# Optimization experiments

Measured on AMD Instinct MI355X. Metric: run time of the kernel, lower is better.

## Reference

```python
import jax, jax.numpy as jnp
import numpy as np

N = 100000   # nodes
E = 3200000  # edges (before self-loops)


def _glorot(k, fi, fo):
    lim = np.sqrt(6.0 / (fi + fo)).astype(np.float32)
    return jax.random.uniform(k, (fi, fo), jnp.float32, -lim, lim)


def setup_inputs() -> dict:
    key = jax.random.key(0)
    ks = jax.random.split(key, 8)
    x = jax.random.normal(ks[0], (N, 128), jnp.float32)
    edge_index = jax.random.randint(ks[1], (2, E), 0, N, dtype=jnp.int32)
    return {
        "x": x,
        "edge_index": edge_index,
        "W1": _glorot(ks[2], 128, 64), "b1": jnp.zeros((64,), jnp.float32),
        "W2": _glorot(ks[3], 64, 32),  "b2": jnp.zeros((32,), jnp.float32),
        "W3": _glorot(ks[4], 32, 16),  "b3": jnp.zeros((16,), jnp.float32),
        "Wl": _glorot(ks[5], 16, 4),   "bl": jnp.zeros((4,), jnp.float32),
    }


def _gcn_layer(h_in, W, b, src, dst, norm, n):
    # PyG GCNConv: x' = D^-1/2 (A+I) D^-1/2 (x W) + b
    h = h_in @ W                                   # [N, out]
    msg = h[src] * norm[:, None]                   # gather + normalize, [E+N, out]
    out = jax.ops.segment_sum(msg, dst, num_segments=n)
    return out + b


def reference(x, edge_index, W1, b1, W2, b2, W3, b3, Wl, bl):
    n = x.shape[0]
    loops = jnp.arange(n, dtype=edge_index.dtype)
    src = jnp.concatenate([edge_index[0], loops])  # source nodes (messages flow src->dst)
    dst = jnp.concatenate([edge_index[1], loops])
    # symmetric gcn_norm with self-loops (edge_weight = 1)
    deg = jax.ops.segment_sum(jnp.ones_like(dst, dtype=x.dtype), dst, num_segments=n)
    dinv = jnp.where(deg > 0, jax.lax.rsqrt(deg), 0.0)
    norm = dinv[src] * dinv[dst]                   # [E+N]

    h = jax.nn.relu(_gcn_layer(x, W1, b1, src, dst, norm, n))
    h = jax.nn.relu(_gcn_layer(h, W2, b2, src, dst, norm, n))
    h = jax.nn.relu(_gcn_layer(h, W3, b3, src, dst, norm, n))
    z = h @ Wl + bl
    return (h, z)
```

## Files before the change

### kernel.cpp

```cpp
#include <hip/hip_runtime.h>

static constexpr int BLK = 256;
static constexpr int BW_SHIFT = 8;
static constexpr int NBUCK_MAX = 512;
static constexpr int CAP = 12288;


__device__ inline float bflo(unsigned u) {
    union { unsigned x; float f; } c; c.x = u << 16; return c.f;
}
__device__ inline float bfhi(unsigned u) {
    union { unsigned x; float f; } c; c.x = u & 0xFFFF0000u; return c.f;
}
__device__ inline unsigned short f2bf(float f) {
    union { float f; unsigned u; } c; c.f = f;
    unsigned u = c.u;
    return (unsigned short)((u + 0x7FFFu + ((u >> 16) & 1u)) >> 16);
}
__device__ inline unsigned pack2(float a, float b) {
    return (unsigned)f2bf(a) | ((unsigned)f2bf(b) << 16);
}


__global__ __launch_bounds__(1024) void k_part(
        const int* __restrict__ src, const int* __restrict__ dst,
        int* __restrict__ bcur, int* __restrict__ pairs, int e, int nbuck) {
    __shared__ int hcnt[NBUCK_MAX];
    __shared__ int hbase[NBUCK_MAX];
    const int nt = blockDim.x;
    int nblk = gridDim.x;
    int per = (e + nblk - 1) / nblk;
    int lo = blockIdx.x * per, hi = min(e, lo + per);
    for (int i = threadIdx.x; i < nbuck; i += nt) hcnt[i] = 0;
    __syncthreads();
    for (int i = lo + threadIdx.x; i < hi; i += nt)
        atomicAdd(&hcnt[dst[i] >> BW_SHIFT], 1);
    __syncthreads();
    for (int i = threadIdx.x; i < nbuck; i += nt) {
        int c = hcnt[i];
        hbase[i] = c ? atomicAdd(bcur + i, c) : 0;
        hcnt[i] = 0;
    }
    __syncthreads();
    for (int i = lo + threadIdx.x; i < hi; i += nt) {
        int d = dst[i];
        int b = d >> BW_SHIFT;
        int pos = hbase[b] + atomicAdd(&hcnt[b], 1);
        if (pos < CAP)
            pairs[(size_t)b * CAP + pos] = src[i] | ((d & 255) << 24);
    }
}


__global__ void k_bktscan(const int* __restrict__ bcur, int* __restrict__ bktbase,
                          int* __restrict__ row_ptr, int nbuck, int n, int e) {
    __shared__ int s[512];
    int v = ((int)threadIdx.x < nbuck) ? bcur[threadIdx.x] : 0;
    s[threadIdx.x] = v;
    __syncthreads();
    for (int off = 1; off < 512; off <<= 1) {
        int t = (threadIdx.x >= (unsigned)off) ? s[threadIdx.x - off] : 0;
        __syncthreads();
        s[threadIdx.x] += t;
        __syncthreads();
    }
    if ((int)threadIdx.x < nbuck)
        bktbase[threadIdx.x] = s[threadIdx.x] - v;
    if (threadIdx.x == 0) row_ptr[n] = e;
}


__global__ __launch_bounds__(512) void k_bucket_build(
        const int* __restrict__ pairs, const int* __restrict__ bcur,
        const int* __restrict__ bktbase, int* __restrict__ row_ptr,
        float* __restrict__ dinv, int* __restrict__ csr, int n) {
    __shared__ int lcnt[256];
    __shared__ int sexc[256];
    const int b = blockIdx.x;
    const int node0 = b << BW_SHIFT;
    const int nn = min(256, n - node0);
    const int cnt = min(bcur[b], CAP);
    const int base = bktbase[b];
    const int* bp = pairs + (size_t)b * CAP;
    const int tid = threadIdx.x;
    const int nt = blockDim.x;

    if (tid < 256) lcnt[tid] = 0;
    __syncthreads();
    for (int i = tid; i < cnt; i += nt)
        atomicAdd(&lcnt[(unsigned)bp[i] >> 24], 1);
    __syncthreads();
    int c = 0;
    if (tid < 256) {
        c = lcnt[tid];
        sexc[tid] = c;
    }
    __syncthreads();
    for (int off = 1; off < 256; off <<= 1) {
        int t = 0;
        if (tid < 256 && tid >= off) t = sexc[tid - off];
        __syncthreads();
        if (tid < 256) sexc[tid] += t;
        __syncthreads();
    }
    if (tid < nn) {
        int excl = sexc[tid] - c;
        row_ptr[node0 + tid] = base + excl;
        dinv[node0 + tid] = rsqrtf((float)(c + 1));
    }
    __syncthreads();
    if (tid < 256) {
        sexc[tid] -= c;
        lcnt[tid] = 0;
    }
    __syncthreads();
    for (int i = tid; i < cnt; i += nt) {
        int pv = bp[i];
        int ld = (unsigned)pv >> 24;
        int pos = base + sexc[ld] + atomicAdd(&lcnt[ld], 1);
        csr[pos] = pv & 0xFFFFFF;
    }
}


template <int K, int F>
__global__ __launch_bounds__(256) void k_gemm_tiled(const float* __restrict__ X,
                                                    const float* __restrict__ W,
                                                    const float* __restrict__ dinv,
                                                    unsigned short* __restrict__ G,
                                                    int n) {
    constexpr int KT = 32;
    constexpr int TF = F / 16;
    static_assert(K % KT == 0, "");
    __shared__ float xs[KT][68];
    __shared__ float wsm[KT * F];
    const int tid = threadIdx.x;
    const int ng = tid & 15;
    const int fg = tid >> 4;
    const int node0 = blockIdx.x * 64;

    float acc[4][TF];
#pragma unroll
    for (int m = 0; m < 4; ++m)
#pragma unroll
        for (int j = 0; j < TF; ++j) acc[m][j] = 0.0f;

    for (int kt = 0; kt < K / KT; ++kt) {
#pragma unroll
        for (int v = 0; v < 2; ++v) {
            int fi = tid + v * 256;
            int nd = fi >> 3, kq = fi & 7;
            int row = min(node0 + nd, n - 1);
            float4 xv = *(const float4*)&X[(size_t)row * K + kt * KT + kq * 4];
            xs[kq * 4 + 0][nd] = xv.x;
            xs[kq * 4 + 1][nd] = xv.y;
            xs[kq * 4 + 2][nd] = xv.z;
            xs[kq * 4 + 3][nd] = xv.w;
        }
        constexpr int WV = KT * F / 4;
        for (int fi = tid; fi < WV; fi += 256)
            ((float4*)wsm)[fi] = ((const float4*)(W + (size_t)kt * KT * F))[fi];
        __syncthreads();

#pragma unroll 8
        for (int kk = 0; kk < KT; ++kk) {
            float4 xv = *(const float4*)&xs[kk][ng * 4];
            float wv[TF];
#pragma unroll
            for (int j = 0; j < TF; ++j) wv[j] = wsm[kk * F + fg * TF + j];
            const float xm[4] = {xv.x, xv.y, xv.z, xv.w};
#pragma unroll
            for (int m = 0; m < 4; ++m)
#pragma unroll
                for (int j = 0; j < TF; ++j) acc[m][j] = fmaf(xm[m], wv[j], acc[m][j]);
        }
        __syncthreads();
    }

#pragma unroll
    for (int m = 0; m < 4; ++m) {
        int node = node0 + ng * 4 + m;
        if (node < n) {
            float di = dinv[node];
            unsigned short* gp = G + (size_t)node * F + fg * TF;
            if constexpr (TF == 4) {
                uint2 o;
                o.x = pack2(acc[m][0] * di, acc[m][1] * di);
                o.y = pack2(acc[m][2] * di, acc[m][3] * di);
                *(uint2*)gp = o;
            } else if constexpr (TF == 2) {
                *(unsigned*)gp = pack2(acc[m][0] * di, acc[m][1] * di);
            } else {
                gp[0] = f2bf(acc[m][0] * di);
            }
        }
    }
}


template <int F, bool HEAD>
__global__ void k_agg(const int* __restrict__ row_ptr, const int* __restrict__ csr,
                      const uint4* __restrict__ g4, const float* __restrict__ dinv,
                      const float* __restrict__ b, float* __restrict__ out, int n,
                      const float* __restrict__ Wl, const float* __restrict__ blp,
                      float* __restrict__ z_out) {
    constexpr int L = F / 8;
    constexpr int NPB = BLK / L;
    __shared__ float wl_s[68];
    if constexpr (HEAD) {
        if (threadIdx.x < 68)
            wl_s[threadIdx.x] = (threadIdx.x < 64) ? Wl[threadIdx.x]
                                                   : blp[threadIdx.x - 64];
        __syncthreads();
    }
    int node = blockIdx.x * NPB + (int)(threadIdx.x / L);
    int q = threadIdx.x % L;
    if (node >= n) return;
    int i = row_ptr[node], end = row_ptr[node + 1];
    float a[8];
#pragma unroll
    for (int j = 0; j < 8; ++j) a[j] = 0.0f;
    for (; i + 3 < end; i += 4) {
        int s0 = csr[i], s1 = csr[i + 1], s2 = csr[i + 2], s3 = csr[i + 3];
        uint4 v0 = g4[(size_t)s0 * L + q];
        uint4 v1 = g4[(size_t)s1 * L + q];
        uint4 v2 = g4[(size_t)s2 * L + q];
        uint4 v3 = g4[(size_t)s3 * L + q];
        a[0] += (bflo(v0.x) + bflo(v1.x)) + (bflo(v2.x) + bflo(v3.x));
        a[1] += (bfhi(v0.x) + bfhi(v1.x)) + (bfhi(v2.x) + bfhi(v3.x));
        a[2] += (bflo(v0.y) + bflo(v1.y)) + (bflo(v2.y) + bflo(v3.y));
        a[3] += (bfhi(v0.y) + bfhi(v1.y)) + (bfhi(v2.y) + bfhi(v3.y));
        a[4] += (bflo(v0.z) + bflo(v1.z)) + (bflo(v2.z) + bflo(v3.z));
        a[5] += (bfhi(v0.z) + bfhi(v1.z)) + (bfhi(v2.z) + bfhi(v3.z));
        a[6] += (bflo(v0.w) + bflo(v1.w)) + (bflo(v2.w) + bflo(v3.w));
        a[7] += (bfhi(v0.w) + bfhi(v1.w)) + (bfhi(v2.w) + bfhi(v3.w));
    }
    for (; i < end; ++i) {
        uint4 v = g4[(size_t)csr[i] * L + q];
        a[0] += bflo(v.x); a[1] += bfhi(v.x);
        a[2] += bflo(v.y); a[3] += bfhi(v.y);
        a[4] += bflo(v.z); a[5] += bfhi(v.z);
        a[6] += bflo(v.w); a[7] += bfhi(v.w);
    }
    uint4 vs = g4[(size_t)node * L + q];
    a[0] += bflo(vs.x); a[1] += bfhi(vs.x);
    a[2] += bflo(vs.y); a[3] += bfhi(vs.y);
    a[4] += bflo(vs.z); a[5] += bfhi(vs.z);
    a[6] += bflo(vs.w); a[7] += bfhi(vs.w);

    float di = dinv[node];
    float4 b0 = ((const float4*)b)[2 * q];
    float4 b1 = ((const float4*)b)[2 * q + 1];
    float h[8];
    h[0] = fmaxf(fmaf(di, a[0], b0.x), 0.0f);
    h[1] = fmaxf(fmaf(di, a[1], b0.y), 0.0f);
    h[2] = fmaxf(fmaf(di, a[2], b0.z), 0.0f);
    h[3] = fmaxf(fmaf(di, a[3], b0.w), 0.0f);
    h[4] = fmaxf(fmaf(di, a[4], b1.x), 0.0f);
    h[5] = fmaxf(fmaf(di, a[5], b1.y), 0.0f);
    h[6] = fmaxf(fmaf(di, a[6], b1.z), 0.0f);
    h[7] = fmaxf(fmaf(di, a[7], b1.w), 0.0f);
    float4* op = (float4*)out + (size_t)node * (F / 4) + 2 * q;
    op[0] = make_float4(h[0], h[1], h[2], h[3]);
    op[1] = make_float4(h[4], h[5], h[6], h[7]);

    if constexpr (HEAD) {
        float p[4];
#pragma unroll
        for (int j = 0; j < 4; ++j) p[j] = 0.0f;
#pragma unroll
        for (int k = 0; k < 8; ++k) {
            const float hv = h[k];
            const int kr = (q * 8 + k) * 4;
#pragma unroll
            for (int j = 0; j < 4; ++j) p[j] = fmaf(hv, wl_s[kr + j], p[j]);
        }
#pragma unroll
        for (int j = 0; j < 4; ++j) p[j] += __shfl_xor(p[j], 1);
        if (q == 0) {
            float4 zt = make_float4(p[0] + wl_s[64], p[1] + wl_s[65],
                                    p[2] + wl_s[66], p[3] + wl_s[67]);
            ((float4*)z_out)[node] = zt;
        }
    }
}


extern "C" void kernel_launch(void* const* d_in, const int* in_sizes, int n_in,
                              void* d_out, int out_size, void* d_ws, size_t ws_size,
                              hipStream_t stream) {
    const float* x  = (const float*)d_in[0];
    const int*   ei = (const int*)d_in[1];
    const float* W1 = (const float*)d_in[2];
    const float* b1 = (const float*)d_in[3];
    const float* W2 = (const float*)d_in[4];
    const float* b2 = (const float*)d_in[5];
    const float* W3 = (const float*)d_in[6];
    const float* b3 = (const float*)d_in[7];
    const float* Wl = (const float*)d_in[8];
    const float* bl = (const float*)d_in[9];

    const int n = in_sizes[0] / 128;
    const int e = in_sizes[1] / 2;
    const int* src = ei;
    const int* dst = ei + e;

    const int nbuck = (n + (1 << BW_SHIFT) - 1) >> BW_SHIFT;

    char* ws = (char*)d_ws;
    size_t off = 0;
    auto alloc = [&](size_t bytes) {
        char* p = ws + off;
        off += (bytes + 255) & ~(size_t)255;
        return p;
    };
    int*   bcur    = (int*)alloc(NBUCK_MAX * 4);
    int*   bktbase = (int*)alloc(NBUCK_MAX * 4);
    int*   row_ptr = (int*)alloc(((size_t)n + 1) * 4);
    float* dinv    = (float*)alloc((size_t)n * 4);
    int*   csr     = (int*)alloc((size_t)e * 4);
    unsigned short* gbuf = (unsigned short*)alloc((size_t)n * 64 * 2);
    float* hbuf    = (float*)alloc((size_t)n * 64 * 4);
    int* pairs = (int*)hbuf;

    float* h_out = (float*)d_out;
    float* z_out = (float*)d_out + (size_t)n * 16;

    hipMemsetAsync(bcur, 0, NBUCK_MAX * 4, stream);
    k_part<<<256, 1024, 0, stream>>>(src, dst, bcur, pairs, e, nbuck);
    k_bktscan<<<1, 512, 0, stream>>>(bcur, bktbase, row_ptr, nbuck, n, e);
    k_bucket_build<<<nbuck, 512, 0, stream>>>(pairs, bcur, bktbase, row_ptr, dinv, csr, n);

    k_gemm_tiled<128, 64><<<(n + 63) / 64, 256, 0, stream>>>(x, W1, dinv, gbuf, n);
    k_agg<64, false><<<(n + 31) / 32, BLK, 0, stream>>>(row_ptr, csr, (const uint4*)gbuf,
                                                        dinv, b1, hbuf, n, nullptr, nullptr, nullptr);

    k_gemm_tiled<64, 32><<<(n + 63) / 64, 256, 0, stream>>>(hbuf, W2, dinv, gbuf, n);
    k_agg<32, false><<<(n + 63) / 64, BLK, 0, stream>>>(row_ptr, csr, (const uint4*)gbuf,
                                                        dinv, b2, hbuf, n, nullptr, nullptr, nullptr);

    k_gemm_tiled<32, 16><<<(n + 63) / 64, 256, 0, stream>>>(hbuf, W3, dinv, gbuf, n);
    k_agg<16, true><<<(n + 127) / 128, BLK, 0, stream>>>(row_ptr, csr, (const uint4*)gbuf,
                                                         dinv, b3, h_out, n, Wl, bl, z_out);
}
```

Measured before the change: 353.4 us.

## Use bf16 MFMA for first-layer GEMM with pre-transposed bf16 weights

Replaces the fp32 FMA tiled GEMM for layer one (128->64) with a kernel that converts X rows to bf16 in swizzled LDS and computes the product with 16x16x32 bf16 MFMA instructions. A small prep kernel transposes W1 to bf16 once per call. This targets the ALU cost of the largest dense GEMM. In exchange, inputs are rounded to bf16 before multiplying, which adds precision loss, and the output stores become scattered 2-byte writes.

```diff
diff --git a/kernel.cpp b/kernel.cpp
--- a/kernel.cpp
+++ b/kernel.cpp
@@ -4,6 +4,9 @@
 static constexpr int BW_SHIFT = 8;
 static constexpr int NBUCK_MAX = 512;
 static constexpr int CAP = 12288;
+
+typedef __attribute__((ext_vector_type(8))) short bf16x8;
+typedef __attribute__((ext_vector_type(4))) float f32x4;
 
 
 __device__ inline float bflo(unsigned u) {
@@ -119,6 +122,99 @@
         int ld = (unsigned)pv >> 24;
         int pos = base + sexc[ld] + atomicAdd(&lcnt[ld], 1);
         csr[pos] = pv & 0xFFFFFF;
+    }
+}
+
+
+__global__ void k_prep_w(const float* __restrict__ W, unsigned short* __restrict__ WT) {
+    int t = blockIdx.x * blockDim.x + threadIdx.x;
+    if (t >= 64 * 128) return;
+    int nf = t >> 7, k = t & 127;
+    WT[t] = f2bf(W[k * 64 + nf]);
+}
+
+
+__global__ __launch_bounds__(256) void k_gemm1_mfma(
+        const float* __restrict__ X, const unsigned short* __restrict__ WT,
+        const float* __restrict__ dinv, unsigned short* __restrict__ G, int n) {
+    __shared__ unsigned short A_lds[64 * 128];
+    __shared__ unsigned short B_lds[64 * 128];
+    const int tid = threadIdx.x;
+    const int node0 = blockIdx.x * 64;
+
+    {
+        const uint4* srcp = (const uint4*)WT;
+#pragma unroll
+        for (int v = 0; v < 4; ++v) {
+            int idx = tid * 4 + v;
+            int r = idx >> 4;
+            int bo = (idx & 15) * 16;
+            uint4 d = srcp[idx];
+            *(uint4*)((char*)B_lds + r * 256 + (bo ^ ((r & 7) << 4))) = d;
+        }
+    }
+    {
+        int nd = tid & 63, kq = tid >> 6;
+        int row = min(node0 + nd, n - 1);
+        const float4* xr = (const float4*)(X + (size_t)row * 128 + kq * 32);
+#pragma unroll
+        for (int v = 0; v < 4; ++v) {
+            float4 f0 = xr[2 * v], f1 = xr[2 * v + 1];
+            uint4 d;
+            d.x = pack2(f0.x, f0.y); d.y = pack2(f0.z, f0.w);
+            d.z = pack2(f1.x, f1.y); d.w = pack2(f1.z, f1.w);
+            int bo = kq * 64 + v * 16;
+            *(uint4*)((char*)A_lds + nd * 256 + (bo ^ ((nd & 7) << 4))) = d;
+        }
+    }
+    __syncthreads();
+
+    const int lane = tid & 63;
+    const int w = tid >> 6;
+    const int lm = lane & 15;
+    const int lk = lane >> 4;
+
+    f32x4 acc0 = {0, 0, 0, 0}, acc1 = {0, 0, 0, 0};
+    f32x4 acc2 = {0, 0, 0, 0}, acc3 = {0, 0, 0, 0};
+
+#pragma unroll
+    for (int ks = 0; ks < 4; ++ks) {
+        const int kbo = ks * 64 + lk * 16;
+        const int ar = w * 16 + lm;
+        bf16x8 a = *(bf16x8*)((char*)A_lds + ar * 256 + (kbo ^ ((ar & 7) << 4)));
+        {
+            const int br = 0 * 16 + lm;
+            bf16x8 b = *(bf16x8*)((char*)B_lds + br * 256 + (kbo ^ ((br & 7) << 4)));
+            acc0 = __builtin_amdgcn_mfma_f32_16x16x32_bf16(a, b, acc0, 0, 0, 0);
+        }
+        {
+            const int br = 1 * 16 + lm;
+            bf16x8 b = *(bf16x8*)((char*)B_lds + br * 256 + (kbo ^ ((br & 7) << 4)));
+            acc1 = __builtin_amdgcn_mfma_f32_16x16x32_bf16(a, b, acc1, 0, 0, 0);
+        }
+        {
+            const int br = 2 * 16 + lm;
+            bf16x8 b = *(bf16x8*)((char*)B_lds + br * 256 + (kbo ^ ((br & 7) << 4)));
+            acc2 = __builtin_amdgcn_mfma_f32_16x16x32_bf16(a, b, acc2, 0, 0, 0);
+        }
+        {
+            const int br = 3 * 16 + lm;
+            bf16x8 b = *(bf16x8*)((char*)B_lds + br * 256 + (kbo ^ ((br & 7) << 4)));
+            acc3 = __builtin_amdgcn_mfma_f32_16x16x32_bf16(a, b, acc3, 0, 0, 0);
+        }
+    }
+
+#pragma unroll
+    for (int r = 0; r < 4; ++r) {
+        int node = node0 + w * 16 + lk * 4 + r;
+        if (node < n) {
+            float di = dinv[node];
+            unsigned short* gp = G + (size_t)node * 64 + lm;
+            gp[0]  = f2bf(acc0[r] * di);
+            gp[16] = f2bf(acc1[r] * di);
+            gp[32] = f2bf(acc2[r] * di);
+            gp[48] = f2bf(acc3[r] * di);
+        }
     }
 }
 
@@ -183,12 +279,7 @@
         if (node < n) {
             float di = dinv[node];
             unsigned short* gp = G + (size_t)node * F + fg * TF;
-            if constexpr (TF == 4) {
-                uint2 o;
-                o.x = pack2(acc[m][0] * di, acc[m][1] * di);
-                o.y = pack2(acc[m][2] * di, acc[m][3] * di);
-                *(uint2*)gp = o;
-            } else if constexpr (TF == 2) {
+            if constexpr (TF == 2) {
                 *(unsigned*)gp = pack2(acc[m][0] * di, acc[m][1] * di);
             } else {
                 gp[0] = f2bf(acc[m][0] * di);
@@ -318,6 +409,7 @@
     int*   bktbase = (int*)alloc(NBUCK_MAX * 4);
     int*   row_ptr = (int*)alloc(((size_t)n + 1) * 4);
     float* dinv    = (float*)alloc((size_t)n * 4);
+    unsigned short* w1t = (unsigned short*)alloc(64 * 128 * 2);
     int*   csr     = (int*)alloc((size_t)e * 4);
     unsigned short* gbuf = (unsigned short*)alloc((size_t)n * 64 * 2);
     float* hbuf    = (float*)alloc((size_t)n * 64 * 4);
@@ -327,11 +419,12 @@
     float* z_out = (float*)d_out + (size_t)n * 16;
 
     hipMemsetAsync(bcur, 0, NBUCK_MAX * 4, stream);
+    k_prep_w<<<32, 256, 0, stream>>>(W1, w1t);
     k_part<<<256, 1024, 0, stream>>>(src, dst, bcur, pairs, e, nbuck);
     k_bktscan<<<1, 512, 0, stream>>>(bcur, bktbase, row_ptr, nbuck, n, e);
     k_bucket_build<<<nbuck, 512, 0, stream>>>(pairs, bcur, bktbase, row_ptr, dinv, csr, n);
 
-    k_gemm_tiled<128, 64><<<(n + 63) / 64, 256, 0, stream>>>(x, W1, dinv, gbuf, n);
+    k_gemm1_mfma<<<(n + 63) / 64, 256, 0, stream>>>(x, w1t, dinv, gbuf, n);
     k_agg<64, false><<<(n + 31) / 32, BLK, 0, stream>>>(row_ptr, csr, (const uint4*)gbuf,
                                                         dinv, b1, hbuf, n, nullptr, nullptr, nullptr);
 
```

Result: faster. 346.5 us (-2.0%).
